# Performance work log

Hardware: AMD Instinct MI355X
Metric: run time of the kernel (lower is better)

## Reference

```python
import jax, jax.numpy as jnp
import numpy as np

D_MODEL = 1024
N_HEADS = 16
D_K = D_MODEL // N_HEADS
MAX_SEQ = 2048
THETA = 10000.0


def _make_cos_sin():
    # cos_sin[i, k, 0] = cos(i / theta**(2k/d_k)), [.., 1] = sin(...)
    pos = np.arange(MAX_SEQ, dtype=np.float32)[:, None]
    k = np.arange(D_K // 2, dtype=np.float32)[None, :]
    ang = pos / (THETA ** (2.0 * k / D_K))
    return jnp.asarray(np.stack([np.cos(ang), np.sin(ang)], axis=-1), dtype=jnp.float32)


def setup_inputs() -> dict:
    key = jax.random.key(0)
    ks = jax.random.split(key, 5)
    std = 2.0 / (D_MODEL + D_MODEL)
    def w(k):
        return std * jax.random.truncated_normal(k, -3.0, 3.0, (D_MODEL, D_MODEL), dtype=jnp.float32)
    return {
        "x": jax.random.normal(ks[0], (4, 2048, D_MODEL), dtype=jnp.float32),
        "Wq": w(ks[1]),
        "Wk": w(ks[2]),
        "Wv": w(ks[3]),
        "Wo": w(ks[4]),
        "cos_sin": _make_cos_sin(),
        "token_positions": jnp.arange(2048, dtype=jnp.int32),
    }


def _rope(x, cos_sin, pos):
    # x: [B, H, S, d_k]; rotate consecutive pairs
    B, H, S, d = x.shape
    xt = x.reshape(B, H, S, d // 2, 2)
    cos = cos_sin[pos, :, 0]  # [S, d/2]
    sin = cos_sin[pos, :, 1]
    x0, x1 = xt[..., 0], xt[..., 1]
    r0 = cos * x0 - sin * x1
    r1 = sin * x0 + cos * x1
    return jnp.stack([r0, r1], axis=-1).reshape(B, H, S, d)


def reference(x, Wq, Wk, Wv, Wo, cos_sin, token_positions):
    B, S, D = x.shape
    H, d = N_HEADS, D_K
    def proj(W):
        y = jnp.einsum('bsi,oi->bso', x, W)
        return y.reshape(B, S, H, d).transpose(0, 2, 1, 3)  # [B,H,S,d]
    q = _rope(proj(Wq), cos_sin, token_positions)
    k = _rope(proj(Wk), cos_sin, token_positions)
    v = proj(Wv)
    scores = jnp.einsum('bhqd,bhkd->bhqk', q, k) / jnp.sqrt(jnp.float32(d))
    causal = jnp.tril(jnp.ones((S, S), dtype=bool))
    scores = jnp.where(causal, scores, -jnp.inf)
    attn = jax.nn.softmax(scores, axis=-1)
    out = jnp.einsum('bhqk,bhkd->bhqd', attn, v)
    out = out.transpose(0, 2, 1, 3).reshape(B, S, D)
    return jnp.einsum('bsi,oi->bso', out, Wo)
```

## Files before the change

### kernel.cpp

```cpp
#include <hip/hip_runtime.h>

constexpr int B_  = 4;
constexpr int S_  = 2048;
constexpr int D_  = 1024;
constexpr int H_  = 16;
constexpr int DK_ = 64;
constexpr int M_  = B_ * S_;

typedef __attribute__((ext_vector_type(8))) short short8;
typedef __attribute__((ext_vector_type(4))) float f32x4;
typedef __attribute__((ext_vector_type(4))) unsigned short us4;

__device__ __forceinline__ unsigned short f2b(float f) {
  unsigned int u = __float_as_uint(f);
  u += 0x7FFFu + ((u >> 16) & 1u);
  return (unsigned short)(u >> 16);
}
__device__ __forceinline__ float b2f(unsigned short h) {
  return __uint_as_float(((unsigned int)h) << 16);
}
__device__ __forceinline__ unsigned int cvtpk(float lo, float hi) {
  unsigned int w;
  asm("v_cvt_pk_bf16_f32 %0, %1, %2" : "=v"(w) : "v"(lo), "v"(hi));
  return w;
}
__device__ __forceinline__ float exp2v(float x) {
  float r;
  asm("v_exp_f32 %0, %1" : "=v"(r) : "v"(x));
  return r;
}

#define GLOAD16(g, l) __builtin_amdgcn_global_load_lds( \
    (const __attribute__((address_space(1))) unsigned int*)(g), \
    (__attribute__((address_space(3))) unsigned int*)(l), 16, 0, 0)

__global__ __launch_bounds__(256) void conv_kernel(
    const float* __restrict__ x,
    const float* __restrict__ wq, const float* __restrict__ wk, const float* __restrict__ wv,
    unsigned short* __restrict__ xb, unsigned short* __restrict__ wb)
{
  const int NX4 = (M_ * D_) / 4;
  const int NW4 = (3 * D_ * D_) / 4;
  int stride = gridDim.x * blockDim.x;
  for (int i = blockIdx.x * blockDim.x + threadIdx.x; i < NX4 + NW4; i += stride) {
    const float4* src; unsigned short* dst; int o;
    if (i < NX4) { src = (const float4*)x; dst = xb; o = i; }
    else {
      int wi = i - NX4;
      int mat = wi >> 18;
      o = wi & 262143;
      src = (const float4*)(mat == 0 ? wq : (mat == 1 ? wk : wv));
      dst = wb + mat * (D_ * D_);
    }
    float4 v = src[o];
    us4 r; r.x = f2b(v.x); r.y = f2b(v.y); r.z = f2b(v.z); r.w = f2b(v.w);
    *(us4*)(dst + o * 4) = r;
  }
}

__global__ __launch_bounds__(256) void conv_wo_kernel(
    const float* __restrict__ wo, unsigned short* __restrict__ wob)
{
  int i = blockIdx.x * 256 + threadIdx.x;
  float4 v = ((const float4*)wo)[i];
  us4 r; r.x = f2b(v.x); r.y = f2b(v.y); r.z = f2b(v.z); r.w = f2b(v.w);
  *(us4*)(wob + i * 4) = r;
}

__global__ __launch_bounds__(256, 2) void gemm_qkv_kernel(
    const unsigned short* __restrict__ xb,
    const unsigned short* __restrict__ wb,
    const float* __restrict__ cs,
    const int* __restrict__ pos,
    unsigned short* __restrict__ qb,
    unsigned short* __restrict__ kb,
    unsigned short* __restrict__ vtb)
{
  __shared__ unsigned short As[2][128 * 64];
  __shared__ unsigned short Bs[2][128 * 64];
  const int tid  = threadIdx.x;
  const int lane = tid & 63;
  const int wid  = tid >> 6;
  const int wm = wid >> 1, wn = wid & 1;
  const int m0 = blockIdx.x * 128;
  const int n0 = blockIdx.y * 128;
  const int l15 = lane & 15, l4 = lane >> 4;
  const int swz7 = l15 & 7;

  int srow[4], sgcc[4], slds[4];
  #pragma unroll
  for (int j = 0; j < 4; ++j) {
    int c = tid + j * 256;
    srow[j] = c >> 3;
    int cc  = c & 7;
    sgcc[j] = cc ^ (srow[j] & 7);
    slds[j] = (wid * 64 + j * 256) * 8;
  }

  f32x4 acc[4][4] = {};

  #pragma unroll
  for (int j = 0; j < 4; ++j) {
    GLOAD16(xb + (m0 + srow[j]) * D_ + sgcc[j] * 8, &As[0][slds[j]]);
    GLOAD16(wb + (n0 + srow[j]) * D_ + sgcc[j] * 8, &Bs[0][slds[j]]);
  }
  __syncthreads();

  for (int t = 0; t < 16; ++t) {
    const int cur = t & 1, nxt = cur ^ 1;
    if (t < 15) {
      const int kcol = (t + 1) * 64;
      #pragma unroll
      for (int j = 0; j < 4; ++j) {
        GLOAD16(xb + (m0 + srow[j]) * D_ + kcol + sgcc[j] * 8, &As[nxt][slds[j]]);
        GLOAD16(wb + (n0 + srow[j]) * D_ + kcol + sgcc[j] * 8, &Bs[nxt][slds[j]]);
      }
    }
    const unsigned short* Ab = &As[cur][0];
    const unsigned short* Bb = &Bs[cur][0];
    #pragma unroll
    for (int ks = 0; ks < 2; ++ks) {
      const int cc = (ks * 4 + l4) ^ swz7;
      short8 af[4], bfr[4];
      #pragma unroll
      for (int mi = 0; mi < 4; ++mi) af[mi]  = *(const short8*)&Ab[(wm*64 + mi*16 + l15)*64 + cc*8];
      #pragma unroll
      for (int ni = 0; ni < 4; ++ni) bfr[ni] = *(const short8*)&Bb[(wn*64 + ni*16 + l15)*64 + cc*8];
      __builtin_amdgcn_s_setprio(1);
      #pragma unroll
      for (int mi = 0; mi < 4; ++mi)
        #pragma unroll
        for (int ni = 0; ni < 4; ++ni)
          acc[mi][ni] = __builtin_amdgcn_mfma_f32_16x16x32_bf16(af[mi], bfr[ni], acc[mi][ni], 0, 0, 0);
      __builtin_amdgcn_s_setprio(0);
    }
    __syncthreads();
  }

  const int bidx = m0 >> 11;
  const int sbase = (m0 & 2047) + wm * 64;

  if (n0 < 2048) {
    unsigned short* dst = (n0 < 1024) ? qb : kb;
    const int nn0 = n0 & 1023;
    const float2* cs2 = (const float2*)cs;
    const float sg = (l15 & 1) ? 1.0f : -1.0f;
    #pragma unroll
    for (int mi = 0; mi < 4; ++mi)
      #pragma unroll
      for (int j = 0; j < 4; ++j) {
        int s = sbase + mi*16 + l4*4 + j;
        int p = pos[s];
        #pragma unroll
        for (int ni = 0; ni < 4; ++ni) {
          int col = nn0 + wn*64 + ni*16 + l15;
          int h = col >> 6, dd = col & 63;
          float val = acc[mi][ni][j];
          float par = __shfl_xor(val, 1);
          float2 cv = cs2[p*32 + (dd >> 1)];
          float r = fmaf(cv.x, val, sg * cv.y * par);
          dst[((bidx*H_ + h)*S_ + s)*DK_ + dd] = f2b(r);
        }
      }
  } else {
    const int nn0 = n0 & 1023;
    const int hB = (nn0 + wn*64) >> 6;
    #pragma unroll
    for (int mi = 0; mi < 4; ++mi) {
      int s4 = sbase + mi*16 + l4*4;
      #pragma unroll
      for (int ni = 0; ni < 4; ++ni) {
        int dd = ni*16 + l15;
        uint2 w;
        w.x = cvtpk(acc[mi][ni][0], acc[mi][ni][1]);
        w.y = cvtpk(acc[mi][ni][2], acc[mi][ni][3]);
        *(uint2*)(vtb + ((bidx*H_ + hB)*DK_ + dd)*S_ + s4) = w;
      }
    }
  }
}

__global__ __launch_bounds__(256, 4) void attn_kernel(
    const unsigned short* __restrict__ qb,
    const unsigned short* __restrict__ kb,
    const unsigned short* __restrict__ vtb,
    unsigned short* __restrict__ ao)
{
  __shared__ unsigned short Ks[64][72];
  __shared__ unsigned short Vs[64][72];
  __shared__ unsigned short Ps[4][16][72];
  const int tid = threadIdx.x, lane = tid & 63, wid = tid >> 6;
  const int l15 = lane & 15, l4 = lane >> 4;

  const int id  = blockIdx.x;
  const int xcd = id & 7, jj2 = id >> 3;
  const int bh  = xcd * 8 + (jj2 & 7);
  const int qt  = 15 - (jj2 >> 3);
  const int q0  = qt * 128;
  const int nkt = 2 * qt + 2;

  const unsigned short* qp = qb  + bh * S_ * DK_;
  const unsigned short* kp = kb  + bh * S_ * DK_;
  const unsigned short* vp = vtb + bh * DK_ * S_;
  const int bidx = bh >> 4, h = bh & 15;

  const float QSC = 0.18033688f;
  short8 qf[2][2];
  #pragma unroll
  for (int y = 0; y < 2; ++y)
    #pragma unroll
    for (int kbk = 0; kbk < 2; ++kbk) {
      short8 raw = *(const short8*)(qp + (q0 + y*64 + wid*16 + l15)*DK_ + kbk*32 + l4*8);
      #pragma unroll
      for (int i = 0; i < 8; ++i) {
        float f = b2f((unsigned short)raw[i]) * QSC;
        raw[i] = (short)f2b(f);
      }
      qf[y][kbk] = raw;
    }

  f32x4 oacc[2][4] = {};
  float mrun[2] = {-1e30f, -1e30f}, lrun[2] = {0.0f, 0.0f};

  short8 kv[2], vv[2];
  #pragma unroll
  for (int jj = 0; jj < 2; ++jj) {
    int c = tid + jj * 256;
    int r = c >> 3, col = (c & 7) * 8;
    kv[jj] = *(const short8*)(kp + r*DK_ + col);
    vv[jj] = *(const short8*)(vp + r*S_ + col);
  }

  for (int kt = 0; kt < nkt; ++kt) {
    __syncthreads();
    #pragma unroll
    for (int jj = 0; jj < 2; ++jj) {
      int c = tid + jj * 256;
      int r = c >> 3, col = (c & 7) * 8;
      *(short8*)&Ks[r][col] = kv[jj];
      *(short8*)&Vs[r][col] = vv[jj];
    }
    __syncthreads();

    if (kt + 1 < nkt) {
      #pragma unroll
      for (int jj = 0; jj < 2; ++jj) {
        int c = tid + jj * 256;
        int r = c >> 3, col = (c & 7) * 8;
        kv[jj] = *(const short8*)(kp + ((kt+1)*64 + r)*DK_ + col);
        vv[jj] = *(const short8*)(vp + r*S_ + (kt+1)*64 + col);
      }
    }

    #pragma unroll
    for (int y = 0; y < 2; ++y) {
      if (kt > 2*qt + y) continue;

      f32x4 sc[4];
      __builtin_amdgcn_s_setprio(1);
      #pragma unroll
      for (int nb = 0; nb < 4; ++nb) {
        short8 k0 = *(const short8*)&Ks[nb*16 + l15][l4*8];
        short8 k1 = *(const short8*)&Ks[nb*16 + l15][32 + l4*8];
        f32x4 z = {};
        z = __builtin_amdgcn_mfma_f32_16x16x32_bf16(k0, qf[y][0], z, 0, 0, 0);
        z = __builtin_amdgcn_mfma_f32_16x16x32_bf16(k1, qf[y][1], z, 0, 0, 0);
        sc[nb] = z;
      }
      __builtin_amdgcn_s_setprio(0);

      if (kt == 2*qt + y) {
        const int qg = q0 + y*64 + wid*16 + l15;
        #pragma unroll
        for (int nb = 0; nb < 4; ++nb)
          #pragma unroll
          for (int j = 0; j < 4; ++j) {
            int kg = kt*64 + nb*16 + l4*4 + j;
            if (kg > qg) sc[nb][j] = -1e30f;
          }
      }

      float tm = sc[0][0];
      #pragma unroll
      for (int nb = 0; nb < 4; ++nb)
        #pragma unroll
        for (int j = 0; j < 4; ++j) tm = fmaxf(tm, sc[nb][j]);
      tm = fmaxf(tm, __shfl_xor(tm, 16));
      tm = fmaxf(tm, __shfl_xor(tm, 32));
      if (!__all(tm - mrun[y] <= 8.0f)) {
        float mnew = fmaxf(mrun[y], tm);
        float corr = exp2v(mrun[y] - mnew);
        mrun[y] = mnew;
        lrun[y] *= corr;
        #pragma unroll
        for (int j = 0; j < 4; ++j) {
          float cj = __shfl(corr, l4*4 + j);
          #pragma unroll
          for (int nb = 0; nb < 4; ++nb) oacc[y][nb][j] *= cj;
        }
      }
      float rs = 0.0f;
      #pragma unroll
      for (int nb = 0; nb < 4; ++nb)
        #pragma unroll
        for (int j = 0; j < 4; ++j) {
          float p = exp2v(sc[nb][j] - mrun[y]);
          sc[nb][j] = p;
          rs += p;
        }
      rs += __shfl_xor(rs, 16);
      rs += __shfl_xor(rs, 32);
      lrun[y] += rs;

      #pragma unroll
      for (int nb = 0; nb < 4; ++nb) {
        uint2 w;
        w.x = cvtpk(sc[nb][0], sc[nb][1]);
        w.y = cvtpk(sc[nb][2], sc[nb][3]);
        *(uint2*)&Ps[wid][l15][nb*16 + l4*4] = w;
      }
      asm volatile("s_waitcnt lgkmcnt(0)" ::: "memory");
      short8 pa0 = *(const short8*)&Ps[wid][l15][l4*8];
      short8 pa1 = *(const short8*)&Ps[wid][l15][32 + l4*8];

      __builtin_amdgcn_s_setprio(1);
      #pragma unroll
      for (int nb = 0; nb < 4; ++nb) {
        short8 v0 = *(const short8*)&Vs[nb*16 + l15][l4*8];
        short8 v1 = *(const short8*)&Vs[nb*16 + l15][32 + l4*8];
        oacc[y][nb] = __builtin_amdgcn_mfma_f32_16x16x32_bf16(pa0, v0, oacc[y][nb], 0, 0, 0);
        oacc[y][nb] = __builtin_amdgcn_mfma_f32_16x16x32_bf16(pa1, v1, oacc[y][nb], 0, 0, 0);
      }
      __builtin_amdgcn_s_setprio(0);
    }
  }

  #pragma unroll
  for (int y = 0; y < 2; ++y)
    #pragma unroll
    for (int j = 0; j < 4; ++j) {
      float lj = __shfl(lrun[y], l4*4 + j);
      float inv = 1.0f / lj;
      int row = q0 + y*64 + wid*16 + l4*4 + j;
      #pragma unroll
      for (int nb = 0; nb < 4; ++nb) {
        int dim = nb*16 + l15;
        ao[((bidx*S_ + row)*H_ + h)*DK_ + dim] = f2b(oacc[y][nb][j] * inv);
      }
    }
}

__global__ __launch_bounds__(256, 2) void gemm_out_kernel(
    const unsigned short* __restrict__ ao,
    const unsigned short* __restrict__ wob,
    float* __restrict__ out)
{
  __shared__ unsigned short As[2][128 * 64];
  __shared__ unsigned short Bs[2][128 * 64];
  const int tid = threadIdx.x, lane = tid & 63, wid = tid >> 6;
  const int wm = wid >> 1, wn = wid & 1;
  const int m0 = blockIdx.x * 128, n0 = blockIdx.y * 128;
  const int l15 = lane & 15, l4 = lane >> 4;
  const int swz7 = l15 & 7;

  int srow[4], sgcc[4], slds[4];
  #pragma unroll
  for (int j = 0; j < 4; ++j) {
    int c = tid + j * 256;
    srow[j] = c >> 3;
    int cc  = c & 7;
    sgcc[j] = cc ^ (srow[j] & 7);
    slds[j] = (wid * 64 + j * 256) * 8;
  }

  f32x4 acc[4][4] = {};

  #pragma unroll
  for (int j = 0; j < 4; ++j) {
    GLOAD16(ao  + (m0 + srow[j]) * D_ + sgcc[j] * 8, &As[0][slds[j]]);
    GLOAD16(wob + (n0 + srow[j]) * D_ + sgcc[j] * 8, &Bs[0][slds[j]]);
  }
  __syncthreads();

  for (int t = 0; t < 16; ++t) {
    const int cur = t & 1, nxt = cur ^ 1;
    if (t < 15) {
      const int kcol = (t + 1) * 64;
      #pragma unroll
      for (int j = 0; j < 4; ++j) {
        GLOAD16(ao  + (m0 + srow[j]) * D_ + kcol + sgcc[j] * 8, &As[nxt][slds[j]]);
        GLOAD16(wob + (n0 + srow[j]) * D_ + kcol + sgcc[j] * 8, &Bs[nxt][slds[j]]);
      }
    }
    const unsigned short* Ab = &As[cur][0];
    const unsigned short* Bb = &Bs[cur][0];
    #pragma unroll
    for (int ks = 0; ks < 2; ++ks) {
      const int cc = (ks * 4 + l4) ^ swz7;
      short8 af[4], bfr[4];
      #pragma unroll
      for (int mi = 0; mi < 4; ++mi) af[mi]  = *(const short8*)&Ab[(wm*64 + mi*16 + l15)*64 + cc*8];
      #pragma unroll
      for (int ni = 0; ni < 4; ++ni) bfr[ni] = *(const short8*)&Bb[(wn*64 + ni*16 + l15)*64 + cc*8];
      __builtin_amdgcn_s_setprio(1);
      #pragma unroll
      for (int mi = 0; mi < 4; ++mi)
        #pragma unroll
        for (int ni = 0; ni < 4; ++ni)
          acc[mi][ni] = __builtin_amdgcn_mfma_f32_16x16x32_bf16(af[mi], bfr[ni], acc[mi][ni], 0, 0, 0);
      __builtin_amdgcn_s_setprio(0);
    }
    __syncthreads();
  }

  #pragma unroll
  for (int mi = 0; mi < 4; ++mi)
    #pragma unroll
    for (int ni = 0; ni < 4; ++ni)
      #pragma unroll
      for (int j = 0; j < 4; ++j) {
        int row = m0 + wm*64 + mi*16 + l4*4 + j;
        int col = n0 + wn*64 + ni*16 + l15;
        out[row * D_ + col] = acc[mi][ni][j];
      }
}

extern "C" void kernel_launch(void* const* d_in, const int* in_sizes, int n_in,
                              void* d_out, int out_size, void* d_ws, size_t ws_size,
                              hipStream_t stream)
{
  const float* x  = (const float*)d_in[0];
  const float* wq = (const float*)d_in[1];
  const float* wk = (const float*)d_in[2];
  const float* wv = (const float*)d_in[3];
  const float* wo = (const float*)d_in[4];
  const float* cs = (const float*)d_in[5];
  const int*  pos = (const int*)d_in[6];
  float* out = (float*)d_out;

  unsigned short* xb = (unsigned short*)d_out;
  unsigned short* wb = xb + M_ * D_;

  unsigned short* qb  = (unsigned short*)d_ws;
  unsigned short* kbf = qb  + M_ * D_;
  unsigned short* vtb = kbf + M_ * D_;
  unsigned short* aob = vtb + M_ * D_;
  unsigned short* wob = qb;

  conv_kernel<<<dim3(2048), dim3(256), 0, stream>>>(x, wq, wk, wv, xb, wb);
  gemm_qkv_kernel<<<dim3(64, 24), dim3(256), 0, stream>>>(xb, wb, cs, pos, qb, kbf, vtb);
  attn_kernel<<<dim3(1024), dim3(256), 0, stream>>>(qb, kbf, vtb, aob);
  conv_wo_kernel<<<dim3(1024), dim3(256), 0, stream>>>(wo, wob);
  gemm_out_kernel<<<dim3(64, 8), dim3(256), 0, stream>>>(aob, wob, out);

  (void)in_sizes; (void)n_in; (void)out_size; (void)ws_size;
}
```

Measured before the change: 184.9 us.

## Shrink attention query tile to 64 rows, double grid, swizzle P buffer

```diff
diff --git a/kernel.cpp b/kernel.cpp
--- a/kernel.cpp
+++ b/kernel.cpp
@@ -180,7 +180,7 @@
   }
 }
 
-__global__ __launch_bounds__(256, 4) void attn_kernel(
+__global__ __launch_bounds__(256, 6) void attn_kernel(
     const unsigned short* __restrict__ qb,
     const unsigned short* __restrict__ kb,
     const unsigned short* __restrict__ vtb,
@@ -188,16 +188,16 @@
 {
   __shared__ unsigned short Ks[64][72];
   __shared__ unsigned short Vs[64][72];
-  __shared__ unsigned short Ps[4][16][72];
+  __shared__ unsigned short Ps[4][16][64];
   const int tid = threadIdx.x, lane = tid & 63, wid = tid >> 6;
   const int l15 = lane & 15, l4 = lane >> 4;
 
   const int id  = blockIdx.x;
-  const int xcd = id & 7, jj2 = id >> 3;
-  const int bh  = xcd * 8 + (jj2 & 7);
-  const int qt  = 15 - (jj2 >> 3);
-  const int q0  = qt * 128;
-  const int nkt = 2 * qt + 2;
+  const int xcd = id & 7, rem = id >> 3;
+  const int bh  = xcd * 8 + (rem & 7);
+  const int qt  = 31 - (rem >> 3);
+  const int q0  = qt * 64;
+  const int nkt = qt + 1;
 
   const unsigned short* qp = qb  + bh * S_ * DK_;
   const unsigned short* kp = kb  + bh * S_ * DK_;
@@ -205,22 +205,20 @@
   const int bidx = bh >> 4, h = bh & 15;
 
   const float QSC = 0.18033688f;
-  short8 qf[2][2];
-  #pragma unroll
-  for (int y = 0; y < 2; ++y)
-    #pragma unroll
-    for (int kbk = 0; kbk < 2; ++kbk) {
-      short8 raw = *(const short8*)(qp + (q0 + y*64 + wid*16 + l15)*DK_ + kbk*32 + l4*8);
-      #pragma unroll
-      for (int i = 0; i < 8; ++i) {
-        float f = b2f((unsigned short)raw[i]) * QSC;
-        raw[i] = (short)f2b(f);
-      }
-      qf[y][kbk] = raw;
-    }
-
-  f32x4 oacc[2][4] = {};
-  float mrun[2] = {-1e30f, -1e30f}, lrun[2] = {0.0f, 0.0f};
+  short8 qf[2];
+  #pragma unroll
+  for (int kbk = 0; kbk < 2; ++kbk) {
+    short8 raw = *(const short8*)(qp + (q0 + wid*16 + l15)*DK_ + kbk*32 + l4*8);
+    #pragma unroll
+    for (int i = 0; i < 8; ++i) {
+      float f = b2f((unsigned short)raw[i]) * QSC;
+      raw[i] = (short)f2b(f);
+    }
+    qf[kbk] = raw;
+  }
+
+  f32x4 oacc[4] = {};
+  float mrun = -1e30f, lrun = 0.0f;
 
   short8 kv[2], vv[2];
   #pragma unroll
@@ -252,102 +250,96 @@
       }
     }
 
-    #pragma unroll
-    for (int y = 0; y < 2; ++y) {
-      if (kt > 2*qt + y) continue;
-
-      f32x4 sc[4];
-      __builtin_amdgcn_s_setprio(1);
-      #pragma unroll
-      for (int nb = 0; nb < 4; ++nb) {
-        short8 k0 = *(const short8*)&Ks[nb*16 + l15][l4*8];
-        short8 k1 = *(const short8*)&Ks[nb*16 + l15][32 + l4*8];
-        f32x4 z = {};
-        z = __builtin_amdgcn_mfma_f32_16x16x32_bf16(k0, qf[y][0], z, 0, 0, 0);
-        z = __builtin_amdgcn_mfma_f32_16x16x32_bf16(k1, qf[y][1], z, 0, 0, 0);
-        sc[nb] = z;
-      }
-      __builtin_amdgcn_s_setprio(0);
-
-      if (kt == 2*qt + y) {
-        const int qg = q0 + y*64 + wid*16 + l15;
-        #pragma unroll
-        for (int nb = 0; nb < 4; ++nb)
-          #pragma unroll
-          for (int j = 0; j < 4; ++j) {
-            int kg = kt*64 + nb*16 + l4*4 + j;
-            if (kg > qg) sc[nb][j] = -1e30f;
-          }
-      }
-
-      float tm = sc[0][0];
-      #pragma unroll
-      for (int nb = 0; nb < 4; ++nb)
-        #pragma unroll
-        for (int j = 0; j < 4; ++j) tm = fmaxf(tm, sc[nb][j]);
-      tm = fmaxf(tm, __shfl_xor(tm, 16));
-      tm = fmaxf(tm, __shfl_xor(tm, 32));
-      if (!__all(tm - mrun[y] <= 8.0f)) {
-        float mnew = fmaxf(mrun[y], tm);
-        float corr = exp2v(mrun[y] - mnew);
-        mrun[y] = mnew;
-        lrun[y] *= corr;
-        #pragma unroll
-        for (int j = 0; j < 4; ++j) {
-          float cj = __shfl(corr, l4*4 + j);
-          #pragma unroll
-          for (int nb = 0; nb < 4; ++nb) oacc[y][nb][j] *= cj;
-        }
-      }
-      float rs = 0.0f;
+    f32x4 sc[4];
+    __builtin_amdgcn_s_setprio(1);
+    #pragma unroll
+    for (int nb = 0; nb < 4; ++nb) {
+      short8 k0 = *(const short8*)&Ks[nb*16 + l15][l4*8];
+      short8 k1 = *(const short8*)&Ks[nb*16 + l15][32 + l4*8];
+      f32x4 z = {};
+      z = __builtin_amdgcn_mfma_f32_16x16x32_bf16(k0, qf[0], z, 0, 0, 0);
+      z = __builtin_amdgcn_mfma_f32_16x16x32_bf16(k1, qf[1], z, 0, 0, 0);
+      sc[nb] = z;
+    }
+    __builtin_amdgcn_s_setprio(0);
+
+    if (kt == qt) {
+      const int qg = q0 + wid*16 + l15;
       #pragma unroll
       for (int nb = 0; nb < 4; ++nb)
         #pragma unroll
         for (int j = 0; j < 4; ++j) {
-          float p = exp2v(sc[nb][j] - mrun[y]);
-          sc[nb][j] = p;
-          rs += p;
+          int kg = kt*64 + nb*16 + l4*4 + j;
+          if (kg > qg) sc[nb][j] = -1e30f;
         }
-      rs += __shfl_xor(rs, 16);
-      rs += __shfl_xor(rs, 32);
-      lrun[y] += rs;
-
-      #pragma unroll
-      for (int nb = 0; nb < 4; ++nb) {
-        uint2 w;
-        w.x = cvtpk(sc[nb][0], sc[nb][1]);
-        w.y = cvtpk(sc[nb][2], sc[nb][3]);
-        *(uint2*)&Ps[wid][l15][nb*16 + l4*4] = w;
-      }
-      asm volatile("s_waitcnt lgkmcnt(0)" ::: "memory");
-      short8 pa0 = *(const short8*)&Ps[wid][l15][l4*8];
-      short8 pa1 = *(const short8*)&Ps[wid][l15][32 + l4*8];
-
-      __builtin_amdgcn_s_setprio(1);
-      #pragma unroll
-      for (int nb = 0; nb < 4; ++nb) {
-        short8 v0 = *(const short8*)&Vs[nb*16 + l15][l4*8];
-        short8 v1 = *(const short8*)&Vs[nb*16 + l15][32 + l4*8];
-        oacc[y][nb] = __builtin_amdgcn_mfma_f32_16x16x32_bf16(pa0, v0, oacc[y][nb], 0, 0, 0);
-        oacc[y][nb] = __builtin_amdgcn_mfma_f32_16x16x32_bf16(pa1, v1, oacc[y][nb], 0, 0, 0);
-      }
-      __builtin_amdgcn_s_setprio(0);
-    }
-  }
-
-  #pragma unroll
-  for (int y = 0; y < 2; ++y)
-    #pragma unroll
-    for (int j = 0; j < 4; ++j) {
-      float lj = __shfl(lrun[y], l4*4 + j);
-      float inv = 1.0f / lj;
-      int row = q0 + y*64 + wid*16 + l4*4 + j;
-      #pragma unroll
-      for (int nb = 0; nb < 4; ++nb) {
-        int dim = nb*16 + l15;
-        ao[((bidx*S_ + row)*H_ + h)*DK_ + dim] = f2b(oacc[y][nb][j] * inv);
-      }
-    }
+    }
+
+    float tm = sc[0][0];
+    #pragma unroll
+    for (int nb = 0; nb < 4; ++nb)
+      #pragma unroll
+      for (int j = 0; j < 4; ++j) tm = fmaxf(tm, sc[nb][j]);
+    tm = fmaxf(tm, __shfl_xor(tm, 16));
+    tm = fmaxf(tm, __shfl_xor(tm, 32));
+    if (!__all(tm - mrun <= 8.0f)) {
+      float mnew = fmaxf(mrun, tm);
+      float corr = exp2v(mrun - mnew);
+      mrun = mnew;
+      lrun *= corr;
+      #pragma unroll
+      for (int j = 0; j < 4; ++j) {
+        float cj = __shfl(corr, l4*4 + j);
+        #pragma unroll
+        for (int nb = 0; nb < 4; ++nb) oacc[nb][j] *= cj;
+      }
+    }
+    float rs = 0.0f;
+    #pragma unroll
+    for (int nb = 0; nb < 4; ++nb)
+      #pragma unroll
+      for (int j = 0; j < 4; ++j) {
+        float p = exp2v(sc[nb][j] - mrun);
+        sc[nb][j] = p;
+        rs += p;
+      }
+    rs += __shfl_xor(rs, 16);
+    rs += __shfl_xor(rs, 32);
+    lrun += rs;
+
+    #pragma unroll
+    for (int nb = 0; nb < 4; ++nb) {
+      uint2 w;
+      w.x = cvtpk(sc[nb][0], sc[nb][1]);
+      w.y = cvtpk(sc[nb][2], sc[nb][3]);
+      int g8 = (nb*4 + l4) ^ ((l15 & 7) << 1);
+      *(uint2*)&Ps[wid][l15][g8*4] = w;
+    }
+    asm volatile("s_waitcnt lgkmcnt(0)" ::: "memory");
+    short8 pa0 = *(const short8*)&Ps[wid][l15][(l4       ^ (l15 & 7))*8];
+    short8 pa1 = *(const short8*)&Ps[wid][l15][((4 + l4) ^ (l15 & 7))*8];
+
+    __builtin_amdgcn_s_setprio(1);
+    #pragma unroll
+    for (int nb = 0; nb < 4; ++nb) {
+      short8 v0 = *(const short8*)&Vs[nb*16 + l15][l4*8];
+      short8 v1 = *(const short8*)&Vs[nb*16 + l15][32 + l4*8];
+      oacc[nb] = __builtin_amdgcn_mfma_f32_16x16x32_bf16(pa0, v0, oacc[nb], 0, 0, 0);
+      oacc[nb] = __builtin_amdgcn_mfma_f32_16x16x32_bf16(pa1, v1, oacc[nb], 0, 0, 0);
+    }
+    __builtin_amdgcn_s_setprio(0);
+  }
+
+  #pragma unroll
+  for (int j = 0; j < 4; ++j) {
+    float lj = __shfl(lrun, l4*4 + j);
+    float inv = 1.0f / lj;
+    int row = q0 + wid*16 + l4*4 + j;
+    #pragma unroll
+    for (int nb = 0; nb < 4; ++nb) {
+      int dim = nb*16 + l15;
+      ao[((bidx*S_ + row)*H_ + h)*DK_ + dim] = f2b(oacc[nb][j] * inv);
+    }
+  }
 }
 
 __global__ __launch_bounds__(256, 2) void gemm_out_kernel(
@@ -449,7 +441,7 @@
 
   conv_kernel<<<dim3(2048), dim3(256), 0, stream>>>(x, wq, wk, wv, xb, wb);
   gemm_qkv_kernel<<<dim3(64, 24), dim3(256), 0, stream>>>(xb, wb, cs, pos, qb, kbf, vtb);
-  attn_kernel<<<dim3(1024), dim3(256), 0, stream>>>(qb, kbf, vtb, aob);
+  attn_kernel<<<dim3(2048), dim3(256), 0, stream>>>(qb, kbf, vtb, aob);
   conv_wo_kernel<<<dim3(1024), dim3(256), 0, stream>>>(wo, wob);
   gemm_out_kernel<<<dim3(64, 8), dim3(256), 0, stream>>>(aob, wob, out);
 
```

Result: slower. 205.8 us (+11.3%).

## Double-buffer attention K/V tiles via direct global-to-LDS loads with XOR swizzle

Applied to the files above, without the earlier changes.

```diff
diff --git a/kernel.cpp b/kernel.cpp
--- a/kernel.cpp
+++ b/kernel.cpp
@@ -186,16 +186,17 @@
     const unsigned short* __restrict__ vtb,
     unsigned short* __restrict__ ao)
 {
-  __shared__ unsigned short Ks[64][72];
-  __shared__ unsigned short Vs[64][72];
-  __shared__ unsigned short Ps[4][16][72];
+  __shared__ unsigned short Ks[2][64 * 64];
+  __shared__ unsigned short Vs[2][64 * 64];
+  __shared__ unsigned short Ps[4][16 * 64];
   const int tid = threadIdx.x, lane = tid & 63, wid = tid >> 6;
   const int l15 = lane & 15, l4 = lane >> 4;
+  const int swz7 = l15 & 7;
 
   const int id  = blockIdx.x;
-  const int xcd = id & 7, jj2 = id >> 3;
-  const int bh  = xcd * 8 + (jj2 & 7);
-  const int qt  = 15 - (jj2 >> 3);
+  const int xcd = id & 7, rem = id >> 3;
+  const int bh  = xcd * 8 + (rem & 7);
+  const int qt  = 15 - (rem >> 3);
   const int q0  = qt * 128;
   const int nkt = 2 * qt + 2;
 
@@ -204,6 +205,16 @@
   const unsigned short* vp = vtb + bh * DK_ * S_;
   const int bidx = bh >> 4, h = bh & 15;
 
+  int srow[2], sgcc[2], slds[2];
+  #pragma unroll
+  for (int j = 0; j < 2; ++j) {
+    int c = tid + j * 256;
+    srow[j] = c >> 3;
+    int cc  = c & 7;
+    sgcc[j] = cc ^ (srow[j] & 7);
+    slds[j] = (wid * 64 + j * 256) * 8;
+  }
+
   const float QSC = 0.18033688f;
   short8 qf[2][2];
   #pragma unroll
@@ -222,33 +233,21 @@
   f32x4 oacc[2][4] = {};
   float mrun[2] = {-1e30f, -1e30f}, lrun[2] = {0.0f, 0.0f};
 
-  short8 kv[2], vv[2];
-  #pragma unroll
-  for (int jj = 0; jj < 2; ++jj) {
-    int c = tid + jj * 256;
-    int r = c >> 3, col = (c & 7) * 8;
-    kv[jj] = *(const short8*)(kp + r*DK_ + col);
-    vv[jj] = *(const short8*)(vp + r*S_ + col);
-  }
+  #pragma unroll
+  for (int j = 0; j < 2; ++j) {
+    GLOAD16(kp + srow[j]*DK_ + sgcc[j]*8, &Ks[0][slds[j]]);
+    GLOAD16(vp + srow[j]*S_  + sgcc[j]*8, &Vs[0][slds[j]]);
+  }
+  __syncthreads();
 
   for (int kt = 0; kt < nkt; ++kt) {
-    __syncthreads();
-    #pragma unroll
-    for (int jj = 0; jj < 2; ++jj) {
-      int c = tid + jj * 256;
-      int r = c >> 3, col = (c & 7) * 8;
-      *(short8*)&Ks[r][col] = kv[jj];
-      *(short8*)&Vs[r][col] = vv[jj];
-    }
-    __syncthreads();
-
+    const int cur = kt & 1, nxt = cur ^ 1;
     if (kt + 1 < nkt) {
-      #pragma unroll
-      for (int jj = 0; jj < 2; ++jj) {
-        int c = tid + jj * 256;
-        int r = c >> 3, col = (c & 7) * 8;
-        kv[jj] = *(const short8*)(kp + ((kt+1)*64 + r)*DK_ + col);
-        vv[jj] = *(const short8*)(vp + r*S_ + (kt+1)*64 + col);
+      const int kb0 = (kt + 1) * 64;
+      #pragma unroll
+      for (int j = 0; j < 2; ++j) {
+        GLOAD16(kp + (kb0 + srow[j])*DK_ + sgcc[j]*8, &Ks[nxt][slds[j]]);
+        GLOAD16(vp + srow[j]*S_ + kb0   + sgcc[j]*8, &Vs[nxt][slds[j]]);
       }
     }
 
@@ -260,8 +259,9 @@
       __builtin_amdgcn_s_setprio(1);
       #pragma unroll
       for (int nb = 0; nb < 4; ++nb) {
-        short8 k0 = *(const short8*)&Ks[nb*16 + l15][l4*8];
-        short8 k1 = *(const short8*)&Ks[nb*16 + l15][32 + l4*8];
+        const int rb = (nb*16 + l15) * 64;
+        short8 k0 = *(const short8*)&Ks[cur][rb + ((l4     ^ swz7) * 8)];
+        short8 k1 = *(const short8*)&Ks[cur][rb + (((4+l4) ^ swz7) * 8)];
         f32x4 z = {};
         z = __builtin_amdgcn_mfma_f32_16x16x32_bf16(k0, qf[y][0], z, 0, 0, 0);
         z = __builtin_amdgcn_mfma_f32_16x16x32_bf16(k1, qf[y][1], z, 0, 0, 0);
@@ -317,22 +317,26 @@
         uint2 w;
         w.x = cvtpk(sc[nb][0], sc[nb][1]);
         w.y = cvtpk(sc[nb][2], sc[nb][3]);
-        *(uint2*)&Ps[wid][l15][nb*16 + l4*4] = w;
+        int ch = nb*2 + (l4 >> 1);
+        *(uint2*)&Ps[wid][l15*64 + ((ch ^ swz7) * 8) + (l4 & 1) * 4] = w;
       }
       asm volatile("s_waitcnt lgkmcnt(0)" ::: "memory");
-      short8 pa0 = *(const short8*)&Ps[wid][l15][l4*8];
-      short8 pa1 = *(const short8*)&Ps[wid][l15][32 + l4*8];
+      short8 pa0 = *(const short8*)&Ps[wid][l15*64 + ((l4     ^ swz7) * 8)];
+      short8 pa1 = *(const short8*)&Ps[wid][l15*64 + (((4+l4) ^ swz7) * 8)];
 
       __builtin_amdgcn_s_setprio(1);
       #pragma unroll
       for (int nb = 0; nb < 4; ++nb) {
-        short8 v0 = *(const short8*)&Vs[nb*16 + l15][l4*8];
-        short8 v1 = *(const short8*)&Vs[nb*16 + l15][32 + l4*8];
+        const int rb = (nb*16 + l15) * 64;
+        short8 v0 = *(const short8*)&Vs[cur][rb + ((l4     ^ swz7) * 8)];
+        short8 v1 = *(const short8*)&Vs[cur][rb + (((4+l4) ^ swz7) * 8)];
         oacc[y][nb] = __builtin_amdgcn_mfma_f32_16x16x32_bf16(pa0, v0, oacc[y][nb], 0, 0, 0);
         oacc[y][nb] = __builtin_amdgcn_mfma_f32_16x16x32_bf16(pa1, v1, oacc[y][nb], 0, 0, 0);
       }
       __builtin_amdgcn_s_setprio(0);
     }
+
+    __syncthreads();
   }
 
   #pragma unroll
```

After: 177.8 us. 1.04x faster.
